# Kernel optimization log

Measured on AMD Instinct MI355X. Metric: run time of the kernel, lower is better.

Reference implementation:

```python
import math
import jax, jax.numpy as jnp
import numpy as np

B, T, E, H = 4, 4096, 512, 8
D = E // H
TOP_K = int(3 * math.log(T))  # autocorrelation_factor * log(time_length) = 24


def setup_inputs() -> dict:
    key = jax.random.key(0)
    ks = jax.random.split(key, 9)
    s = 0.02
    return {
        "hidden_states": jax.random.normal(ks[0], (B, T, E), jnp.float32),
        "Wq": jax.random.normal(ks[1], (E, E), jnp.float32) * s,
        "bq": jax.random.normal(ks[2], (E,), jnp.float32) * s,
        "Wk": jax.random.normal(ks[3], (E, E), jnp.float32) * s,
        "bk": jax.random.normal(ks[4], (E,), jnp.float32) * s,
        "Wv": jax.random.normal(ks[5], (E, E), jnp.float32) * s,
        "bv": jax.random.normal(ks[6], (E,), jnp.float32) * s,
        "Wo": jax.random.normal(ks[7], (E, E), jnp.float32) * s,
        "bo": jax.random.normal(ks[8], (E,), jnp.float32) * s,
    }


def _heads(x):
    # [B,T,E] -> [B*H,T,D] (b-major over heads, matching torch view/transpose/reshape)
    return x.reshape(B, T, H, D).transpose(0, 2, 1, 3).reshape(B * H, T, D)


def reference(hidden_states, Wq, bq, Wk, bk, Wv, bv, Wo, bo):
    q = _heads(hidden_states @ Wq.T + bq)
    k = _heads(hidden_states @ Wk.T + bk)
    v = _heads(hidden_states @ Wv.T + bv)

    # FFT-based autocorrelation: irfft(rfft(q) * conj(rfft(k)))  -> [B*H,T,D]
    qf = jnp.fft.rfft(q, n=T, axis=1)
    kf = jnp.fft.rfft(k, n=T, axis=1)
    ac = jnp.fft.irfft(qf * jnp.conj(kf), n=T, axis=1)

    # mean over heads and channels -> [B,T]; eval-mode per-batch top-k delays
    ac_mean = ac.reshape(B, H, T, D).mean(axis=(1, 3))
    top_vals, top_idx = jax.lax.top_k(ac_mean, TOP_K)      # [B,K]
    w = jax.nn.softmax(top_vals, axis=-1)                  # [B,K]

    # torch .repeat(num_heads,...) tiles batch entries: row j uses batch j % B
    w_t = jnp.tile(w, (H, 1))        # [B*H,K]
    d_t = jnp.tile(top_idx, (H, 1))  # [B*H,K]

    t = jnp.arange(T)
    agg = jnp.zeros_like(v)
    for i in range(TOP_K):
        idx = (t[None, :] + d_t[:, i:i + 1]) % T           # circular shift by -delay
        rolled = jnp.take_along_axis(v, idx[:, :, None], axis=1)
        agg = agg + w_t[:, i][:, None, None] * rolled

    out = agg.reshape(B, H, T, D).transpose(0, 2, 1, 3).reshape(B, T, E)
    return out @ Wo.T + bo
```

## Files before the change

### kernel.cpp

```cpp
#include <hip/hip_runtime.h>
#include <math.h>

#define B_ 4
#define T_ 4096
#define E_ 512
#define H_ 8
#define TOPK 24
#define FH 2049
#define FHP 2064
#define F2 2064
#define ZROWS 16512

typedef __attribute__((ext_vector_type(8))) short bf16x8;
typedef __attribute__((ext_vector_type(4))) short bf16x4;
typedef __attribute__((ext_vector_type(4))) float f32x4;

__device__ __forceinline__ unsigned short f2bf(float f) {
    unsigned u = __float_as_uint(f);
    u = (u + 0x7FFFu + ((u >> 16) & 1u)) >> 16;
    return (unsigned short)u;
}
__device__ __forceinline__ float bf2f(unsigned short h) {
    return __uint_as_float(((unsigned)h) << 16);
}

__global__ __launch_bounds__(256) void trsp_split(const float* __restrict__ hid,
                                                  float* __restrict__ Htr,
                                                  unsigned short* __restrict__ Ah)
{
    __shared__ float tile[64][68];
    const int b = blockIdx.z;
    const int t0 = blockIdx.x * 64, e0 = blockIdx.y * 64;
    const int r = threadIdx.x >> 4;
    const int c4 = (threadIdx.x & 15) * 4;
#pragma unroll
    for (int s = 0; s < 4; s++) {
        int t = t0 + r + 16 * s;
        float4 v = *(const float4*)&hid[((size_t)b * T_ + t) * E_ + e0 + c4];
        tile[r + 16 * s][c4 + 0] = v.x; tile[r + 16 * s][c4 + 1] = v.y;
        tile[r + 16 * s][c4 + 2] = v.z; tile[r + 16 * s][c4 + 3] = v.w;
        ushort4 hv = make_ushort4(f2bf(v.x), f2bf(v.y), f2bf(v.z), f2bf(v.w));
        *(ushort4*)&Ah[((size_t)b * T_ + t) * E_ + e0 + c4] = hv;
    }
    __syncthreads();
#pragma unroll
    for (int s = 0; s < 4; s++) {
        int e = e0 + r + 16 * s;
        float4 o;
        o.x = tile[c4 + 0][r + 16 * s];
        o.y = tile[c4 + 1][r + 16 * s];
        o.z = tile[c4 + 2][r + 16 * s];
        o.w = tile[c4 + 3][r + 16 * s];
        *(float4*)&Htr[((size_t)b * E_ + e) * T_ + t0 + c4] = o;
    }
}

__global__ __launch_bounds__(256) void split_w2(const float* __restrict__ wv,
                                                const float* __restrict__ wo,
                                                unsigned short* __restrict__ Wvh,
                                                unsigned short* __restrict__ Woh)
{
    const float* src = blockIdx.y ? wo : wv;
    unsigned short* dst = blockIdx.y ? Woh : Wvh;
    int i = (blockIdx.x * 256 + threadIdx.x) * 4;
    float4 v = *(const float4*)&src[i];
    *(ushort4*)&dst[i] = make_ushort4(f2bf(v.x), f2bf(v.y), f2bf(v.z), f2bf(v.w));
}

__global__ __launch_bounds__(256) void wprep_partial(const float* __restrict__ Wq,
                                                     const float* __restrict__ Wk,
                                                     float* __restrict__ Mp)
{
    __shared__ float As[8][132];
    __shared__ float Bs[8][132];
    const int j0 = blockIdx.x * 128, k0 = blockIdx.y * 128;
    const int e0 = blockIdx.z * 32;
    const int tid = threadIdx.x;
    const int tm = tid & 15, tn = tid >> 4;
    const int le = tid >> 5, lc = (tid & 31) * 4;
    float acc[8][8];
#pragma unroll
    for (int i = 0; i < 8; i++)
#pragma unroll
        for (int j = 0; j < 8; j++) acc[i][j] = 0.f;
    for (int eb = e0; eb < e0 + 32; eb += 8) {
        __syncthreads();
        *(float4*)&As[le][lc] = *(const float4*)&Wq[((size_t)(eb + le)) * 512 + k0 + lc];
        *(float4*)&Bs[le][lc] = *(const float4*)&Wk[((size_t)(eb + le)) * 512 + j0 + lc];
        __syncthreads();
#pragma unroll
        for (int e = 0; e < 8; e++) {
            float a[8], bb[8];
            *(float4*)&a[0] = *(float4*)&As[e][4 * tn];
            *(float4*)&a[4] = *(float4*)&As[e][64 + 4 * tn];
            *(float4*)&bb[0] = *(float4*)&Bs[e][4 * tm];
            *(float4*)&bb[4] = *(float4*)&Bs[e][64 + 4 * tm];
#pragma unroll
            for (int i = 0; i < 8; i++)
#pragma unroll
                for (int j = 0; j < 8; j++)
                    acc[i][j] += a[i] * bb[j];
        }
    }
    float* out = Mp + (size_t)blockIdx.z * 512 * 512;
#pragma unroll
    for (int jj = 0; jj < 8; jj++) {
        int j = j0 + ((jj < 4) ? (4 * tm + jj) : (64 + 4 * tm + jj - 4));
        float4 o0 = make_float4(acc[0][jj], acc[1][jj], acc[2][jj], acc[3][jj]);
        float4 o1 = make_float4(acc[4][jj], acc[5][jj], acc[6][jj], acc[7][jj]);
        *(float4*)&out[(size_t)j * 512 + k0 + 4 * tn] = o0;
        *(float4*)&out[(size_t)j * 512 + k0 + 64 + 4 * tn] = o1;
    }
}

__global__ __launch_bounds__(256) void reduce_split_m(const float* __restrict__ Mp,
                                                      unsigned short* __restrict__ Mth,
                                                      unsigned short* __restrict__ Mtl)
{
    int i = (blockIdx.x * 256 + threadIdx.x) * 4;
    if (i >= 512 * 512) return;
    float4 s = make_float4(0.f, 0.f, 0.f, 0.f);
#pragma unroll
    for (int z = 0; z < 16; z++) {
        float4 v = *(const float4*)&Mp[(size_t)z * 262144 + i];
        s.x += v.x; s.y += v.y; s.z += v.z; s.w += v.w;
    }
    float f[4] = {s.x, s.y, s.z, s.w};
    unsigned short hh[4], ll[4];
#pragma unroll
    for (int r = 0; r < 4; r++) {
        hh[r] = f2bf(f[r]);
        ll[r] = f2bf(f[r] - bf2f(hh[r]));
    }
    *(ushort4*)&Mth[i] = make_ushort4(hh[0], hh[1], hh[2], hh[3]);
    *(ushort4*)&Mtl[i] = make_ushort4(ll[0], ll[1], ll[2], ll[3]);
}

template<int PASSES, int AMODE, int OMODE, int HASBIAS>
__global__ __launch_bounds__(256) void mfma_gemm(const unsigned short* __restrict__ Ah,
                                                 const unsigned short* __restrict__ Al,
                                                 const unsigned short* __restrict__ Bh,
                                                 const unsigned short* __restrict__ Bl,
                                                 const float* __restrict__ bias,
                                                 void* __restrict__ Cp)
{
    constexpr int ATS = 128 * 40;
    constexpr int BTS = 64 * 40;
    constexpr int TOT = (PASSES == 3) ? 2 * (ATS + BTS) : (ATS + BTS);
    __shared__ short smem[TOT];
    short* At  = smem;
    short* Alt = smem + ((PASSES == 3) ? ATS : 0);
    short* Bt  = smem + ((PASSES == 3) ? 2 * ATS : ATS);
    short* Blt = Bt + ((PASSES == 3) ? BTS : 0);

    const int tid = threadIdx.x;
    const int m0 = blockIdx.x * 64;
    const int n0 = blockIdx.y * 128;
    const int wid = tid >> 6, lane = tid & 63;
    const int wn = wid >> 1, wm = wid & 1;
    const int lr = lane & 15, lg = lane >> 4;
    const int kb = lg * 8;

    f32x4 acc[4][2];
#pragma unroll
    for (int i = 0; i < 4; i++)
#pragma unroll
        for (int j = 0; j < 2; j++) acc[i][j] = (f32x4)0.f;

    const int r0 = tid >> 2, kp = (tid & 3) << 3;

    for (int k0 = 0; k0 < 512; k0 += 32) {
        __syncthreads();
        if (AMODE == 0) {
            size_t a0 = (size_t)(n0 + r0) * 512 + k0 + kp;
            size_t a1 = (size_t)(n0 + r0 + 64) * 512 + k0 + kp;
            *(bf16x8*)&At[r0 * 40 + kp]        = *(const bf16x8*)&Ah[a0];
            *(bf16x8*)&At[(r0 + 64) * 40 + kp] = *(const bf16x8*)&Ah[a1];
            if (PASSES == 3) {
                *(bf16x8*)&Alt[r0 * 40 + kp]        = *(const bf16x8*)&Al[a0];
                *(bf16x8*)&Alt[(r0 + 64) * 40 + kp] = *(const bf16x8*)&Al[a1];
            }
        } else {
            size_t za = (size_t)((k0 + kp) >> 2) * ZROWS;
            const size_t st = (size_t)ZROWS * 4;
            size_t a0 = (za + n0 + r0) * 4;
            size_t a1 = (za + n0 + r0 + 64) * 4;
            *(bf16x4*)&At[r0 * 40 + kp]            = *(const bf16x4*)&Ah[a0];
            *(bf16x4*)&At[r0 * 40 + kp + 4]        = *(const bf16x4*)&Ah[a0 + st];
            *(bf16x4*)&At[(r0 + 64) * 40 + kp]     = *(const bf16x4*)&Ah[a1];
            *(bf16x4*)&At[(r0 + 64) * 40 + kp + 4] = *(const bf16x4*)&Ah[a1 + st];
            if (PASSES == 3) {
                *(bf16x4*)&Alt[r0 * 40 + kp]            = *(const bf16x4*)&Al[a0];
                *(bf16x4*)&Alt[r0 * 40 + kp + 4]        = *(const bf16x4*)&Al[a0 + st];
                *(bf16x4*)&Alt[(r0 + 64) * 40 + kp]     = *(const bf16x4*)&Al[a1];
                *(bf16x4*)&Alt[(r0 + 64) * 40 + kp + 4] = *(const bf16x4*)&Al[a1 + st];
            }
        }
        size_t bb = (size_t)(m0 + r0) * 512 + k0 + kp;
        *(bf16x8*)&Bt[r0 * 40 + kp] = *(const bf16x8*)&Bh[bb];
        if (PASSES == 3)
            *(bf16x8*)&Blt[r0 * 40 + kp] = *(const bf16x8*)&Bl[bb];
        __syncthreads();

        bf16x8 a[4], b[2];
#pragma unroll
        for (int f = 0; f < 4; f++)
            a[f] = *(bf16x8*)&At[(wn * 64 + f * 16 + lr) * 40 + kb];
#pragma unroll
        for (int j = 0; j < 2; j++)
            b[j] = *(bf16x8*)&Bt[(wm * 32 + j * 16 + lr) * 40 + kb];
        if (PASSES == 3) {
            bf16x8 a2[4], b2[2];
#pragma unroll
            for (int f = 0; f < 4; f++)
                a2[f] = *(bf16x8*)&Alt[(wn * 64 + f * 16 + lr) * 40 + kb];
#pragma unroll
            for (int j = 0; j < 2; j++)
                b2[j] = *(bf16x8*)&Blt[(wm * 32 + j * 16 + lr) * 40 + kb];
#pragma unroll
            for (int i = 0; i < 4; i++)
#pragma unroll
                for (int j = 0; j < 2; j++) {
                    acc[i][j] = __builtin_amdgcn_mfma_f32_16x16x32_bf16(a[i], b[j], acc[i][j], 0, 0, 0);
                    acc[i][j] = __builtin_amdgcn_mfma_f32_16x16x32_bf16(a[i], b2[j], acc[i][j], 0, 0, 0);
                    acc[i][j] = __builtin_amdgcn_mfma_f32_16x16x32_bf16(a2[i], b[j], acc[i][j], 0, 0, 0);
                }
        } else {
#pragma unroll
            for (int i = 0; i < 4; i++)
#pragma unroll
                for (int j = 0; j < 2; j++)
                    acc[i][j] = __builtin_amdgcn_mfma_f32_16x16x32_bf16(a[i], b[j], acc[i][j], 0, 0, 0);
        }
    }

    float bs[2];
#pragma unroll
    for (int j = 0; j < 2; j++) bs[j] = HASBIAS ? bias[m0 + wm * 32 + j * 16 + lr] : 0.f;

    if (OMODE == 0) {
        float* C = (float*)Cp;
#pragma unroll
        for (int i = 0; i < 4; i++)
#pragma unroll
            for (int j = 0; j < 2; j++) {
                int m = m0 + wm * 32 + j * 16 + lr;
#pragma unroll
                for (int r = 0; r < 4; r++) {
                    int n = n0 + wn * 64 + i * 16 + lg * 4 + r;
                    C[(size_t)n * 512 + m] = acc[i][j][r] + bs[j];
                }
            }
    } else {
        unsigned short* C = (unsigned short*)Cp;
#pragma unroll
        for (int i = 0; i < 4; i++)
#pragma unroll
            for (int j = 0; j < 2; j++) {
                int m = m0 + wm * 32 + j * 16 + lr;
#pragma unroll
                for (int r = 0; r < 4; r++) {
                    int n = n0 + wn * 64 + i * 16 + lg * 4 + r;
                    C[(size_t)n * 512 + m] = f2bf(acc[i][j][r] + bs[j]);
                }
            }
    }
}

template<int SGN>
__device__ __forceinline__ void radix8(float* xr, float* xi)
{
    const float C = 0.70710678118654752440f;
    const float S = (float)SGN;
    float t0r = xr[0] + xr[4], t0i = xi[0] + xi[4];
    float t1r = xr[1] + xr[5], t1i = xi[1] + xi[5];
    float t2r = xr[2] + xr[6], t2i = xi[2] + xi[6];
    float t3r = xr[3] + xr[7], t3i = xi[3] + xi[7];
    float u0r = xr[0] - xr[4], u0i = xi[0] - xi[4];
    float a1r = xr[1] - xr[5], a1i = xi[1] - xi[5];
    float a2r = xr[2] - xr[6], a2i = xi[2] - xi[6];
    float a3r = xr[3] - xr[7], a3i = xi[3] - xi[7];
    float u1r = C * (a1r - S * a1i), u1i = C * (S * a1r + a1i);
    float u2r = -S * a2i,             u2i = S * a2r;
    float u3r = -C * (a3r + S * a3i), u3i = C * (S * a3r - a3i);
    float v0r = t0r + t2r, v0i = t0i + t2i;
    float w0r = t0r - t2r, w0i = t0i - t2i;
    float v1r = t1r + t3r, v1i = t1i + t3i;
    float w1r = -S * (t1i - t3i), w1i = S * (t1r - t3r);
    float p0r = u0r + u2r, p0i = u0i + u2i;
    float q0r = u0r - u2r, q0i = u0i - u2i;
    float p1r = u1r + u3r, p1i = u1i + u3i;
    float q1r = -S * (u1i - u3i), q1i = S * (u1r - u3r);
    xr[0] = v0r + v1r; xi[0] = v0i + v1i;
    xr[4] = v0r - v1r; xi[4] = v0i - v1i;
    xr[2] = w0r + w1r; xi[2] = w0i + w1i;
    xr[6] = w0r - w1r; xi[6] = w0i - w1i;
    xr[1] = p0r + p1r; xi[1] = p0i + p1i;
    xr[5] = p0r - p1r; xi[5] = p0i - p1i;
    xr[3] = q0r + q1r; xi[3] = q0i + q1i;
    xr[7] = q0r - q1r; xi[7] = q0i - q1i;
}

__device__ __forceinline__ void twmul(float& xr, float& xi, float wc, float ws)
{
    float a = xr, b = xi;
    xr = a * wc - b * ws;
    xi = a * ws + b * wc;
}

__device__ __forceinline__ void twiddle7(float* xr, float* xi, int n, float ang)
{
    float s1, c1;
    __sincosf(ang * (float)n, &s1, &c1);
    float wc = c1, ws = s1;
    twmul(xr[1], xi[1], wc, ws);
#pragma unroll
    for (int r = 2; r < 8; r++) {
        float nc = wc * c1 - ws * s1;
        float ns = wc * s1 + ws * c1;
        wc = nc; ws = ns;
        twmul(xr[r], xi[r], wc, ws);
    }
}

#define SW(i) ((i) + ((i) >> 3))

template<int SGN>
__device__ __forceinline__ void fft_core(float* xr, float* xi,
                                         float* lre, float* lim, int tid)
{
    const float TW = (float)SGN * 6.28318530717958647693f;
    __syncthreads();
    radix8<SGN>(xr, xi);
    twiddle7(xr, xi, tid, TW / 4096.f);
#pragma unroll
    for (int r = 0; r < 8; r++) {
        int idx = r * 512 + tid;
        lre[SW(idx)] = xr[r]; lim[SW(idx)] = xi[r];
    }
    __syncthreads();
    const int b2 = (tid >> 6) * 512, n2 = tid & 63;
#pragma unroll
    for (int s = 0; s < 8; s++) {
        int idx = b2 + n2 + s * 64;
        xr[s] = lre[SW(idx)]; xi[s] = lim[SW(idx)];
    }
    __syncthreads();
    radix8<SGN>(xr, xi);
    twiddle7(xr, xi, n2, TW / 512.f);
#pragma unroll
    for (int r = 0; r < 8; r++) {
        int idx = b2 + r * 64 + n2;
        lre[SW(idx)] = xr[r]; lim[SW(idx)] = xi[r];
    }
    __syncthreads();
    const int b3 = (tid >> 3) * 64, n3 = tid & 7;
#pragma unroll
    for (int s = 0; s < 8; s++) {
        int idx = b3 + n3 + s * 8;
        xr[s] = lre[SW(idx)]; xi[s] = lim[SW(idx)];
    }
    __syncthreads();
    radix8<SGN>(xr, xi);
    twiddle7(xr, xi, n3, TW / 64.f);
#pragma unroll
    for (int r = 0; r < 8; r++) {
        int idx = b3 + r * 8 + n3;
        lre[SW(idx)] = xr[r]; lim[SW(idx)] = xi[r];
    }
    __syncthreads();
#pragma unroll
    for (int s = 0; s < 8; s++) {
        int idx = tid * 8 + s;
        xr[s] = lre[SW(idx)]; xi[s] = lim[SW(idx)];
    }
    __syncthreads();
    radix8<SGN>(xr, xi);
    const int fr = ((tid & 7) << 6) | (((tid >> 3) & 7) << 3) | (tid >> 6);
#pragma unroll
    for (int r = 0; r < 8; r++) {
        int f = r * 512 + fr;
        lre[SW(f)] = xr[r]; lim[SW(f)] = xi[r];
    }
    __syncthreads();
}

__global__ __launch_bounds__(512) void fft_fwd_z(const float* __restrict__ Htr,
                                                 unsigned short* __restrict__ Zh,
                                                 unsigned short* __restrict__ Zl)
{
    __shared__ float lre[4608];
    __shared__ float lim[4608];
    const int bid = blockIdx.x;
    const int tid = threadIdx.x;
    const int b = bid >> 7;
    const int e0 = (bid & 127) * 4;
    const int kbi = e0 >> 2;
    unsigned uh[4][2][2], ul[4][2][2];
#pragma unroll
    for (int p = 0; p < 2; p++) {
        const float* he = Htr + ((size_t)(b * 512 + e0 + 2 * p)) * 4096;
        const float* ho = Htr + ((size_t)(b * 512 + e0 + 2 * p + 1)) * 4096;
        float xr[8], xi[8];
#pragma unroll
        for (int s = 0; s < 8; s++) {
            xr[s] = he[tid + 512 * s];
            xi[s] = ho[tid + 512 * s];
        }
        fft_core<-1>(xr, xi, lre, lim, tid);
#pragma unroll
        for (int s = 0; s < 4; s++) {
            int f = tid + 512 * s;
            int nf = (4096 - f) & 4095;
            float Ax = lre[SW(f)],  Ay = lim[SW(f)];
            float Bx = lre[SW(nf)], By = lim[SW(nf)];
            float qx = 0.5f * (Ax + Bx), qy = 0.5f * (Ay - By);
            float kx = 0.5f * (Ay + By), ky = -0.5f * (Ax - Bx);
            unsigned short h0 = f2bf(qx), h1 = f2bf(kx);
            uh[s][0][p] = (unsigned)h0 | ((unsigned)h1 << 16);
            ul[s][0][p] = (unsigned)f2bf(qx - bf2f(h0)) | ((unsigned)f2bf(kx - bf2f(h1)) << 16);
            unsigned short h2 = f2bf(qy), h3 = f2bf(ky);
            uh[s][1][p] = (unsigned)h2 | ((unsigned)h3 << 16);
            ul[s][1][p] = (unsigned)f2bf(qy - bf2f(h2)) | ((unsigned)f2bf(ky - bf2f(h3)) << 16);
        }
        if (tid == 0) {
            float Ax = lre[SW(2048)], Ay = lim[SW(2048)];
            size_t row0 = (size_t)(b * 2) * F2 + 2048;
            size_t off0 = ((size_t)kbi * ZROWS + row0) * 4 + 2 * p;
            unsigned short h = f2bf(Ax);
            Zh[off0] = h; Zl[off0] = f2bf(Ax - bf2f(h));
            unsigned short h2 = f2bf(Ay);
            Zh[off0 + 1] = h2; Zl[off0 + 1] = f2bf(Ay - bf2f(h2));
            size_t off1 = ((size_t)kbi * ZROWS + row0 + F2) * 4 + 2 * p;
            Zh[off1] = 0; Zl[off1] = 0;
            Zh[off1 + 1] = 0; Zl[off1 + 1] = 0;
        }
    }
#pragma unroll
    for (int s = 0; s < 4; s++)
#pragma unroll
        for (int c = 0; c < 2; c++) {
            size_t row = (size_t)(b * 2 + c) * F2 + tid + 512 * s;
            size_t off = ((size_t)kbi * ZROWS + row) * 4;
            ushort4 vh = make_ushort4((unsigned short)(uh[s][c][0] & 0xffff),
                                      (unsigned short)(uh[s][c][0] >> 16),
                                      (unsigned short)(uh[s][c][1] & 0xffff),
                                      (unsigned short)(uh[s][c][1] >> 16));
            ushort4 vl = make_ushort4((unsigned short)(ul[s][c][0] & 0xffff),
                                      (unsigned short)(ul[s][c][0] >> 16),
                                      (unsigned short)(ul[s][c][1] & 0xffff),
                                      (unsigned short)(ul[s][c][1] >> 16));
            *(ushort4*)&Zh[off] = vh;
            *(ushort4*)&Zl[off] = vl;
        }
}

__global__ __launch_bounds__(256) void dot_s(const float* __restrict__ Y,
                                             const unsigned short* __restrict__ Zh,
                                             const unsigned short* __restrict__ Zl,
                                             float2* __restrict__ Sp)
{
    const int f = blockIdx.x * 256 + threadIdx.x;
    const int b = blockIdx.y;
    const int gz = blockIdx.z;
    if (f > 2048) return;
    const size_t row_re = (size_t)(b * 2) * F2 + f;
    const size_t row_im = row_re + F2;
    float sre = 0.f, sim = 0.f;
    for (int kb = gz * 16; kb < gz * 16 + 16; kb++) {
        size_t zr_off = ((size_t)kb * ZROWS + row_re) * 4;
        size_t zi_off = ((size_t)kb * ZROWS + row_im) * 4;
        bf16x4 zrh = *(const bf16x4*)&Zh[zr_off];
        bf16x4 zrl = *(const bf16x4*)&Zl[zr_off];
        bf16x4 zih = *(const bf16x4*)&Zh[zi_off];
        bf16x4 zil = *(const bf16x4*)&Zl[zi_off];
        float4 yr = *(const float4*)&Y[row_re * 512 + kb * 4];
        float4 yi = *(const float4*)&Y[row_im * 512 + kb * 4];
        float yrv[4] = {yr.x, yr.y, yr.z, yr.w};
        float yiv[4] = {yi.x, yi.y, yi.z, yi.w};
#pragma unroll
        for (int j = 0; j < 4; j++) {
            float zr = bf2f((unsigned short)zrh[j]) + bf2f((unsigned short)zrl[j]);
            float zi = bf2f((unsigned short)zih[j]) + bf2f((unsigned short)zil[j]);
            sre += yrv[j] * zr + yiv[j] * zi;
            sim += yiv[j] * zr - yrv[j] * zi;
        }
    }
    Sp[((size_t)gz * 4 + b) * FHP + f] = make_float2(sre, sim);
}

__global__ __launch_bounds__(512) void ifft_kernel(const float2* __restrict__ Sp,
                                                   float* __restrict__ acm)
{
    __shared__ float lre[4608];
    __shared__ float lim[4608];
    const int b = blockIdx.x, tid = threadIdx.x;
    float xr[8], xi[8];
#pragma unroll
    for (int s = 0; s < 8; s++) {
        int idx = tid + 512 * s;
        int src = (idx <= 2048) ? idx : (4096 - idx);
        float sx = 0.f, sy = 0.f;
#pragma unroll
        for (int gz = 0; gz < 8; gz++) {
            float2 v = Sp[((size_t)gz * 4 + b) * FHP + src];
            sx += v.x; sy += v.y;
        }
        xr[s] = sx;
        xi[s] = (idx <= 2048) ? sy : -sy;
    }
    fft_core<1>(xr, xi, lre, lim, tid);
    const float scale = 1.0f / ((float)T_ * (float)E_);
#pragma unroll
    for (int s = 0; s < 8; s++) {
        int p = tid + 512 * s;
        acm[b * T_ + p] = lre[SW(p)] * scale;
    }
}

__global__ __launch_bounds__(256) void topk_kernel(const float* __restrict__ acm,
                                                   int* __restrict__ delays,
                                                   float* __restrict__ weights)
{
    __shared__ float vals[4096];
    __shared__ float bv[256];
    __shared__ int   bi[256];
    __shared__ float topv[TOPK];
    const int b = blockIdx.x, tid = threadIdx.x;
#pragma unroll
    for (int s = 0; s < 16; s++) vals[tid + 256 * s] = acm[b * T_ + tid + 256 * s];
    __syncthreads();
    for (int it = 0; it < TOPK; it++) {
        float best = -INFINITY; int bidx = 0;
#pragma unroll
        for (int s = 0; s < 16; s++) {
            int idx = tid * 16 + s;
            float v = vals[idx];
            if (v > best) { best = v; bidx = idx; }
        }
        bv[tid] = best; bi[tid] = bidx;
        __syncthreads();
        for (int off = 128; off > 0; off >>= 1) {
            if (tid < off) {
                if (bv[tid + off] > bv[tid] ||
                    (bv[tid + off] == bv[tid] && bi[tid + off] < bi[tid])) {
                    bv[tid] = bv[tid + off]; bi[tid] = bi[tid + off];
                }
            }
            __syncthreads();
        }
        if (tid == 0) {
            delays[b * TOPK + it] = bi[0];
            topv[it] = bv[0];
            vals[bi[0]] = -INFINITY;
        }
        __syncthreads();
    }
    if (tid == 0) {
        float mx = topv[0];
        float w[TOPK], sum = 0.f;
        for (int i = 0; i < TOPK; i++) { w[i] = expf(topv[i] - mx); sum += w[i]; }
        for (int i = 0; i < TOPK; i++) weights[b * TOPK + i] = w[i] / sum;
    }
}

__global__ __launch_bounds__(256) void agg_kernel(const unsigned short* __restrict__ V,
                                                  const int* __restrict__ delays,
                                                  const float* __restrict__ wts,
                                                  unsigned short* __restrict__ agg)
{
    __shared__ int   dly[B_][TOPK];
    __shared__ float wt[B_][TOPK];
    const int tid = threadIdx.x, b = blockIdx.y;
    if (tid < B_ * TOPK) {
        dly[tid / TOPK][tid % TOPK] = delays[tid];
        wt[tid / TOPK][tid % TOPK]  = wts[tid];
    }
    __syncthreads();
    const int lane = tid & 63, w = tid >> 6;
    const int t = blockIdx.x * 4 + w;
    const int e8 = lane * 8;
    const int h = e8 >> 6;
    const int c = (b * H_ + h) % B_;
    const unsigned short* Vb = V + (size_t)b * T_ * E_;
    float acc[8];
#pragma unroll
    for (int j = 0; j < 8; j++) acc[j] = 0.f;
#pragma unroll
    for (int i = 0; i < TOPK; i++) {
        int tt = (t + dly[c][i]) & (T_ - 1);
        bf16x8 v = *(const bf16x8*)&Vb[(size_t)tt * E_ + e8];
        float wg = wt[c][i];
#pragma unroll
        for (int j = 0; j < 8; j++)
            acc[j] += wg * bf2f((unsigned short)v[j]);
    }
    bf16x8 o;
#pragma unroll
    for (int j = 0; j < 8; j++) o[j] = (short)f2bf(acc[j]);
    *(bf16x8*)&agg[((size_t)b * T_ + t) * E_ + e8] = o;
}

extern "C" void kernel_launch(void* const* d_in, const int* in_sizes, int n_in,
                              void* d_out, int out_size, void* d_ws, size_t ws_size,
                              hipStream_t stream)
{
    const float* hidden = (const float*)d_in[0];
    const float* Wq = (const float*)d_in[1];
    const float* Wk = (const float*)d_in[3];
    const float* Wv = (const float*)d_in[5]; const float* bv = (const float*)d_in[6];
    const float* Wo = (const float*)d_in[7]; const float* bo = (const float*)d_in[8];

    char* ws = (char*)d_ws;
    const size_t YA_OFF  = 0;
    const size_t AH_OFF  = 33816576;
    const size_t ZH_OFF  = 50593792;
    const size_t ZL_OFF  = 67502080;
    const size_t VB_OFF  = 84410368;
    const size_t MTH_OFF = 101187584;
    const size_t MTL_OFF = 101711872;
    const size_t WVH_OFF = 102236160;
    const size_t WOH_OFF = 102760448;
    const size_t SP_OFF  = 103284736;
    const size_t ACM_OFF = 103813120;
    const size_t DEL_OFF = 103878656;
    const size_t WTS_OFF = 103879040;
    if (ws_size < 103879424) return;

    float* Htr = (float*)(ws + YA_OFF);
    float* Y   = (float*)(ws + YA_OFF);
    unsigned short* Ah  = (unsigned short*)(ws + AH_OFF);
    unsigned short* Ag  = (unsigned short*)(ws + AH_OFF);
    unsigned short* Zh  = (unsigned short*)(ws + ZH_OFF);
    unsigned short* Zl  = (unsigned short*)(ws + ZL_OFF);
    float* Mp           = (float*)(ws + VB_OFF);
    unsigned short* Vb  = (unsigned short*)(ws + VB_OFF);
    unsigned short* Mth = (unsigned short*)(ws + MTH_OFF);
    unsigned short* Mtl = (unsigned short*)(ws + MTL_OFF);
    unsigned short* Wvh = (unsigned short*)(ws + WVH_OFF);
    unsigned short* Woh = (unsigned short*)(ws + WOH_OFF);
    float2* Sp   = (float2*)(ws + SP_OFF);
    float*  acm  = (float*)(ws + ACM_OFF);
    int*    delays = (int*)(ws + DEL_OFF);
    float*  wts    = (float*)(ws + WTS_OFF);

    dim3 tg(64, 8, 4);
    trsp_split<<<tg, 256, 0, stream>>>(hidden, Htr, Ah);
    dim3 swg(256, 2);
    split_w2<<<swg, 256, 0, stream>>>(Wv, Wo, Wvh, Woh);
    dim3 mg(4, 4, 16);
    wprep_partial<<<mg, 256, 0, stream>>>(Wq, Wk, Mp);
    reduce_split_m<<<256, 256, 0, stream>>>(Mp, Mth, Mtl);

    dim3 gv(8, 128);
    mfma_gemm<1, 0, 2, 1><<<gv, 256, 0, stream>>>(Ah, Ah, Wvh, Wvh, bv, Vb);

    fft_fwd_z<<<512, 512, 0, stream>>>(Htr, Zh, Zl);

    dim3 gy(8, 129);
    mfma_gemm<3, 1, 0, 0><<<gy, 256, 0, stream>>>(Zh, Zl, Mth, Mtl, bv, Y);

    dim3 dg(9, 4, 8);
    dot_s<<<dg, 256, 0, stream>>>(Y, Zh, Zl, Sp);

    ifft_kernel<<<B_, 512, 0, stream>>>(Sp, acm);
    topk_kernel<<<B_, 256, 0, stream>>>(acm, delays, wts);
    dim3 ag(T_ / 4, B_);
    agg_kernel<<<ag, 256, 0, stream>>>(Vb, delays, wts, Ag);
    mfma_gemm<1, 0, 0, 1><<<gv, 256, 0, stream>>>(Ag, Ag, Woh, Woh, bo, (float*)d_out);
}
```

Measured before the change: 285.4 us.

## Use k-chunked operand layout with direct global-to-LDS loads, fuse V and Y GEMMs

All GEMM operands (activations, weights, Z spectra, aggregated values) are rewritten in a k-chunk-major layout of 8 bf16 per row, so GEMM tiles can be filled with global_load_lds 16-byte direct copies instead of register round-trips. The GEMM tile grows from 128x64 to 128x128 with 4x4 MFMA fragments per wave. The V projection and the 3-pass Y GEMM are merged into one launch using blockIdx.z. Producers and dot_s are updated to match the new layout. This aims to reduce LDS staging overhead and launch count, at the cost of more registers per thread and LDS layouts without padding that may cause bank conflicts.

```diff
diff --git a/kernel.cpp b/kernel.cpp
--- a/kernel.cpp
+++ b/kernel.cpp
@@ -10,9 +10,9 @@
 #define FHP 2064
 #define F2 2064
 #define ZROWS 16512
+#define NRH 16384
 
 typedef __attribute__((ext_vector_type(8))) short bf16x8;
-typedef __attribute__((ext_vector_type(4))) short bf16x4;
 typedef __attribute__((ext_vector_type(4))) float f32x4;
 
 __device__ __forceinline__ unsigned short f2bf(float f) {
@@ -23,6 +23,12 @@
 __device__ __forceinline__ float bf2f(unsigned short h) {
     return __uint_as_float(((unsigned)h) << 16);
 }
+__device__ __forceinline__ void glds16(const unsigned short* g, short* l) {
+    __builtin_amdgcn_global_load_lds(
+        (const __attribute__((address_space(1))) unsigned int*)g,
+        (__attribute__((address_space(3))) unsigned int*)l, 16, 0, 0);
+}
+
 
 __global__ __launch_bounds__(256) void trsp_split(const float* __restrict__ hid,
                                                   float* __restrict__ Htr,
@@ -40,7 +46,9 @@
         tile[r + 16 * s][c4 + 0] = v.x; tile[r + 16 * s][c4 + 1] = v.y;
         tile[r + 16 * s][c4 + 2] = v.z; tile[r + 16 * s][c4 + 3] = v.w;
         ushort4 hv = make_ushort4(f2bf(v.x), f2bf(v.y), f2bf(v.z), f2bf(v.w));
-        *(ushort4*)&Ah[((size_t)b * T_ + t) * E_ + e0 + c4] = hv;
+        int e = e0 + c4;
+        int rowg = b * T_ + t;
+        *(ushort4*)&Ah[((size_t)(e >> 3) * NRH + rowg) * 8 + (e & 7)] = hv;
     }
     __syncthreads();
 #pragma unroll
@@ -63,8 +71,10 @@
     const float* src = blockIdx.y ? wo : wv;
     unsigned short* dst = blockIdx.y ? Woh : Wvh;
     int i = (blockIdx.x * 256 + threadIdx.x) * 4;
+    int m = i >> 9, k = i & 511;
     float4 v = *(const float4*)&src[i];
-    *(ushort4*)&dst[i] = make_ushort4(f2bf(v.x), f2bf(v.y), f2bf(v.z), f2bf(v.w));
+    *(ushort4*)&dst[((size_t)(k >> 3) * 512 + m) * 8 + (k & 7)] =
+        make_ushort4(f2bf(v.x), f2bf(v.y), f2bf(v.z), f2bf(v.w));
 }
 
 __global__ __launch_bounds__(256) void wprep_partial(const float* __restrict__ Wq,
@@ -125,6 +135,7 @@
         float4 v = *(const float4*)&Mp[(size_t)z * 262144 + i];
         s.x += v.x; s.y += v.y; s.z += v.z; s.w += v.w;
     }
+    int j = i >> 9, k = i & 511;
     float f[4] = {s.x, s.y, s.z, s.w};
     unsigned short hh[4], ll[4];
 #pragma unroll
@@ -132,95 +143,68 @@
         hh[r] = f2bf(f[r]);
         ll[r] = f2bf(f[r] - bf2f(hh[r]));
     }
-    *(ushort4*)&Mth[i] = make_ushort4(hh[0], hh[1], hh[2], hh[3]);
-    *(ushort4*)&Mtl[i] = make_ushort4(ll[0], ll[1], ll[2], ll[3]);
-}
-
-template<int PASSES, int AMODE, int OMODE, int HASBIAS>
-__global__ __launch_bounds__(256) void mfma_gemm(const unsigned short* __restrict__ Ah,
-                                                 const unsigned short* __restrict__ Al,
-                                                 const unsigned short* __restrict__ Bh,
-                                                 const unsigned short* __restrict__ Bl,
-                                                 const float* __restrict__ bias,
-                                                 void* __restrict__ Cp)
-{
-    constexpr int ATS = 128 * 40;
-    constexpr int BTS = 64 * 40;
-    constexpr int TOT = (PASSES == 3) ? 2 * (ATS + BTS) : (ATS + BTS);
-    __shared__ short smem[TOT];
-    short* At  = smem;
-    short* Alt = smem + ((PASSES == 3) ? ATS : 0);
-    short* Bt  = smem + ((PASSES == 3) ? 2 * ATS : ATS);
-    short* Blt = Bt + ((PASSES == 3) ? BTS : 0);
-
+    size_t o = ((size_t)(k >> 3) * 512 + j) * 8 + (k & 7);
+    *(ushort4*)&Mth[o] = make_ushort4(hh[0], hh[1], hh[2], hh[3]);
+    *(ushort4*)&Mtl[o] = make_ushort4(ll[0], ll[1], ll[2], ll[3]);
+}
+
+template<int PASSES, int OMODE, int HASBIAS>
+__device__ __forceinline__ void gemm_body(const unsigned short* __restrict__ Ah,
+                                          const unsigned short* __restrict__ Al, int nrA,
+                                          const unsigned short* __restrict__ Bh,
+                                          const unsigned short* __restrict__ Bl,
+                                          const float* __restrict__ bias,
+                                          void* __restrict__ Cp,
+                                          int m0, int n0, short* smem)
+{
     const int tid = threadIdx.x;
-    const int m0 = blockIdx.x * 64;
-    const int n0 = blockIdx.y * 128;
     const int wid = tid >> 6, lane = tid & 63;
     const int wn = wid >> 1, wm = wid & 1;
     const int lr = lane & 15, lg = lane >> 4;
-    const int kb = lg * 8;
-
-    f32x4 acc[4][2];
+
+    f32x4 acc[4][4];
 #pragma unroll
     for (int i = 0; i < 4; i++)
 #pragma unroll
-        for (int j = 0; j < 2; j++) acc[i][j] = (f32x4)0.f;
-
-    const int r0 = tid >> 2, kp = (tid & 3) << 3;
-
-    for (int k0 = 0; k0 < 512; k0 += 32) {
+        for (int j = 0; j < 4; j++) acc[i][j] = (f32x4)0.f;
+
+    constexpr int SEGW = (PASSES == 3) ? 8 : 4;
+
+    for (int kc0 = 0; kc0 < 64; kc0 += 4) {
         __syncthreads();
-        if (AMODE == 0) {
-            size_t a0 = (size_t)(n0 + r0) * 512 + k0 + kp;
-            size_t a1 = (size_t)(n0 + r0 + 64) * 512 + k0 + kp;
-            *(bf16x8*)&At[r0 * 40 + kp]        = *(const bf16x8*)&Ah[a0];
-            *(bf16x8*)&At[(r0 + 64) * 40 + kp] = *(const bf16x8*)&Ah[a1];
-            if (PASSES == 3) {
-                *(bf16x8*)&Alt[r0 * 40 + kp]        = *(const bf16x8*)&Al[a0];
-                *(bf16x8*)&Alt[(r0 + 64) * 40 + kp] = *(const bf16x8*)&Al[a1];
+#pragma unroll
+        for (int s = 0; s < SEGW; s++) {
+            const int sg = wid * SEGW + s;
+            const int tile = sg >> 3;
+            const int seg = sg & 7;
+            const int c = seg >> 1, h = seg & 1;
+            const unsigned short* bp;
+            size_t ro;
+            if (tile == 0)      { bp = Ah; ro = (size_t)(kc0 + c) * (size_t)nrA + n0 + h * 64; }
+            else if (tile == 1) { bp = Bh; ro = (size_t)(kc0 + c) * 512 + m0 + h * 64; }
+            else if (tile == 2) { bp = Al; ro = (size_t)(kc0 + c) * (size_t)nrA + n0 + h * 64; }
+            else                { bp = Bl; ro = (size_t)(kc0 + c) * 512 + m0 + h * 64; }
+            glds16(bp + ro * 8 + (size_t)lane * 8, smem + tile * 4096 + seg * 512);
+        }
+        __syncthreads();
+
+        bf16x8 a[4], b[4];
+#pragma unroll
+        for (int f = 0; f < 4; f++) {
+            a[f] = *(bf16x8*)&smem[       (lg * 128 + wn * 64 + f * 16 + lr) * 8];
+            b[f] = *(bf16x8*)&smem[4096 + (lg * 128 + wm * 64 + f * 16 + lr) * 8];
+        }
+        if (PASSES == 3) {
+            bf16x8 a2[4], b2[4];
+#pragma unroll
+            for (int f = 0; f < 4; f++) {
+                a2[f] = *(bf16x8*)&smem[8192  + (lg * 128 + wn * 64 + f * 16 + lr) * 8];
+                b2[f] = *(bf16x8*)&smem[12288 + (lg * 128 + wm * 64 + f * 16 + lr) * 8];
             }
-        } else {
-            size_t za = (size_t)((k0 + kp) >> 2) * ZROWS;
-            const size_t st = (size_t)ZROWS * 4;
-            size_t a0 = (za + n0 + r0) * 4;
-            size_t a1 = (za + n0 + r0 + 64) * 4;
-            *(bf16x4*)&At[r0 * 40 + kp]            = *(const bf16x4*)&Ah[a0];
-            *(bf16x4*)&At[r0 * 40 + kp + 4]        = *(const bf16x4*)&Ah[a0 + st];
-            *(bf16x4*)&At[(r0 + 64) * 40 + kp]     = *(const bf16x4*)&Ah[a1];
-            *(bf16x4*)&At[(r0 + 64) * 40 + kp + 4] = *(const bf16x4*)&Ah[a1 + st];
-            if (PASSES == 3) {
-                *(bf16x4*)&Alt[r0 * 40 + kp]            = *(const bf16x4*)&Al[a0];
-                *(bf16x4*)&Alt[r0 * 40 + kp + 4]        = *(const bf16x4*)&Al[a0 + st];
-                *(bf16x4*)&Alt[(r0 + 64) * 40 + kp]     = *(const bf16x4*)&Al[a1];
-                *(bf16x4*)&Alt[(r0 + 64) * 40 + kp + 4] = *(const bf16x4*)&Al[a1 + st];
-            }
-        }
-        size_t bb = (size_t)(m0 + r0) * 512 + k0 + kp;
-        *(bf16x8*)&Bt[r0 * 40 + kp] = *(const bf16x8*)&Bh[bb];
-        if (PASSES == 3)
-            *(bf16x8*)&Blt[r0 * 40 + kp] = *(const bf16x8*)&Bl[bb];
-        __syncthreads();
-
-        bf16x8 a[4], b[2];
-#pragma unroll
-        for (int f = 0; f < 4; f++)
-            a[f] = *(bf16x8*)&At[(wn * 64 + f * 16 + lr) * 40 + kb];
-#pragma unroll
-        for (int j = 0; j < 2; j++)
-            b[j] = *(bf16x8*)&Bt[(wm * 32 + j * 16 + lr) * 40 + kb];
-        if (PASSES == 3) {
-            bf16x8 a2[4], b2[2];
-#pragma unroll
-            for (int f = 0; f < 4; f++)
-                a2[f] = *(bf16x8*)&Alt[(wn * 64 + f * 16 + lr) * 40 + kb];
-#pragma unroll
-            for (int j = 0; j < 2; j++)
-                b2[j] = *(bf16x8*)&Blt[(wm * 32 + j * 16 + lr) * 40 + kb];
 #pragma unroll
             for (int i = 0; i < 4; i++)
 #pragma unroll
-                for (int j = 0; j < 2; j++) {
+                for (int j = 0; j < 4; j++) {
                     acc[i][j] = __builtin_amdgcn_mfma_f32_16x16x32_bf16(a[i], b[j], acc[i][j], 0, 0, 0);
                     acc[i][j] = __builtin_amdgcn_mfma_f32_16x16x32_bf16(a[i], b2[j], acc[i][j], 0, 0, 0);
                     acc[i][j] = __builtin_amdgcn_mfma_f32_16x16x32_bf16(a2[i], b[j], acc[i][j], 0, 0, 0);
@@ -229,22 +213,22 @@
 #pragma unroll
             for (int i = 0; i < 4; i++)
 #pragma unroll
-                for (int j = 0; j < 2; j++)
+                for (int j = 0; j < 4; j++)
                     acc[i][j] = __builtin_amdgcn_mfma_f32_16x16x32_bf16(a[i], b[j], acc[i][j], 0, 0, 0);
         }
     }
 
-    float bs[2];
-#pragma unroll
-    for (int j = 0; j < 2; j++) bs[j] = HASBIAS ? bias[m0 + wm * 32 + j * 16 + lr] : 0.f;
+    float bs[4];
+#pragma unroll
+    for (int j = 0; j < 4; j++) bs[j] = HASBIAS ? bias[m0 + wm * 64 + j * 16 + lr] : 0.f;
 
     if (OMODE == 0) {
         float* C = (float*)Cp;
 #pragma unroll
         for (int i = 0; i < 4; i++)
 #pragma unroll
-            for (int j = 0; j < 2; j++) {
-                int m = m0 + wm * 32 + j * 16 + lr;
+            for (int j = 0; j < 4; j++) {
+                int m = m0 + wm * 64 + j * 16 + lr;
 #pragma unroll
                 for (int r = 0; r < 4; r++) {
                     int n = n0 + wn * 64 + i * 16 + lg * 4 + r;
@@ -256,8 +240,8 @@
 #pragma unroll
         for (int i = 0; i < 4; i++)
 #pragma unroll
-            for (int j = 0; j < 2; j++) {
-                int m = m0 + wm * 32 + j * 16 + lr;
+            for (int j = 0; j < 4; j++) {
+                int m = m0 + wm * 64 + j * 16 + lr;
 #pragma unroll
                 for (int r = 0; r < 4; r++) {
                     int n = n0 + wn * 64 + i * 16 + lg * 4 + r;
@@ -265,6 +249,36 @@
                 }
             }
     }
+}
+
+__global__ __launch_bounds__(256) void fused_vy(const unsigned short* __restrict__ Ah,
+                                                const unsigned short* __restrict__ Wvh,
+                                                const float* __restrict__ bv,
+                                                unsigned short* __restrict__ Vb,
+                                                const unsigned short* __restrict__ Zh,
+                                                const unsigned short* __restrict__ Zl,
+                                                const unsigned short* __restrict__ Mth,
+                                                const unsigned short* __restrict__ Mtl,
+                                                float* __restrict__ Y)
+{
+    __shared__ short smem[16384];
+    const int m0 = blockIdx.x * 128;
+    const int n0 = blockIdx.y * 128;
+    if (blockIdx.z == 0) {
+        if (blockIdx.y >= 128) return;
+        gemm_body<1, 2, 1>(Ah, Ah, NRH, Wvh, Wvh, bv, Vb, m0, n0, smem);
+    } else {
+        gemm_body<3, 0, 0>(Zh, Zl, ZROWS, Mth, Mtl, nullptr, Y, m0, n0, smem);
+    }
+}
+
+__global__ __launch_bounds__(256) void o_gemm(const unsigned short* __restrict__ Ag,
+                                              const unsigned short* __restrict__ Woh,
+                                              const float* __restrict__ bo,
+                                              float* __restrict__ C)
+{
+    __shared__ short smem[8192];
+    gemm_body<1, 0, 1>(Ag, Ag, NRH, Woh, Woh, bo, C, blockIdx.x * 128, blockIdx.y * 128, smem);
 }
 
 template<int SGN>
@@ -395,7 +409,6 @@
     const int tid = threadIdx.x;
     const int b = bid >> 7;
     const int e0 = (bid & 127) * 4;
-    const int kbi = e0 >> 2;
     unsigned uh[4][2][2], ul[4][2][2];
 #pragma unroll
     for (int p = 0; p < 2; p++) {
@@ -424,16 +437,17 @@
             ul[s][1][p] = (unsigned)f2bf(qy - bf2f(h2)) | ((unsigned)f2bf(ky - bf2f(h3)) << 16);
         }
         if (tid == 0) {
-            float Ax = lre[SW(2048)], Ay = lim[SW(2048)];
+            float vals[2] = {lre[SW(2048)], lim[SW(2048)]};
             size_t row0 = (size_t)(b * 2) * F2 + 2048;
-            size_t off0 = ((size_t)kbi * ZROWS + row0) * 4 + 2 * p;
-            unsigned short h = f2bf(Ax);
-            Zh[off0] = h; Zl[off0] = f2bf(Ax - bf2f(h));
-            unsigned short h2 = f2bf(Ay);
-            Zh[off0 + 1] = h2; Zl[off0 + 1] = f2bf(Ay - bf2f(h2));
-            size_t off1 = ((size_t)kbi * ZROWS + row0 + F2) * 4 + 2 * p;
-            Zh[off1] = 0; Zl[off1] = 0;
-            Zh[off1 + 1] = 0; Zl[off1 + 1] = 0;
+#pragma unroll
+            for (int q = 0; q < 2; q++) {
+                int e = e0 + 2 * p + q;
+                size_t o0 = ((size_t)(e >> 3) * ZROWS + row0) * 8 + (e & 7);
+                unsigned short h = f2bf(vals[q]);
+                Zh[o0] = h; Zl[o0] = f2bf(vals[q] - bf2f(h));
+                size_t o1 = ((size_t)(e >> 3) * ZROWS + row0 + F2) * 8 + (e & 7);
+                Zh[o1] = 0; Zl[o1] = 0;
+            }
         }
     }
 #pragma unroll
@@ -441,7 +455,7 @@
 #pragma unroll
         for (int c = 0; c < 2; c++) {
             size_t row = (size_t)(b * 2 + c) * F2 + tid + 512 * s;
-            size_t off = ((size_t)kbi * ZROWS + row) * 4;
+            size_t off = ((size_t)(e0 >> 3) * ZROWS + row) * 8 + (e0 & 7);
             ushort4 vh = make_ushort4((unsigned short)(uh[s][c][0] & 0xffff),
                                       (unsigned short)(uh[s][c][0] >> 16),
                                       (unsigned short)(uh[s][c][1] & 0xffff),
@@ -467,19 +481,19 @@
     const size_t row_re = (size_t)(b * 2) * F2 + f;
     const size_t row_im = row_re + F2;
     float sre = 0.f, sim = 0.f;
-    for (int kb = gz * 16; kb < gz * 16 + 16; kb++) {
-        size_t zr_off = ((size_t)kb * ZROWS + row_re) * 4;
-        size_t zi_off = ((size_t)kb * ZROWS + row_im) * 4;
-        bf16x4 zrh = *(const bf16x4*)&Zh[zr_off];
-        bf16x4 zrl = *(const bf16x4*)&Zl[zr_off];
-        bf16x4 zih = *(const bf16x4*)&Zh[zi_off];
-        bf16x4 zil = *(const bf16x4*)&Zl[zi_off];
-        float4 yr = *(const float4*)&Y[row_re * 512 + kb * 4];
-        float4 yi = *(const float4*)&Y[row_im * 512 + kb * 4];
-        float yrv[4] = {yr.x, yr.y, yr.z, yr.w};
-        float yiv[4] = {yi.x, yi.y, yi.z, yi.w};
-#pragma unroll
-        for (int j = 0; j < 4; j++) {
+    for (int c = gz * 8; c < gz * 8 + 8; c++) {
+        bf16x8 zrh = *(const bf16x8*)&Zh[((size_t)c * ZROWS + row_re) * 8];
+        bf16x8 zrl = *(const bf16x8*)&Zl[((size_t)c * ZROWS + row_re) * 8];
+        bf16x8 zih = *(const bf16x8*)&Zh[((size_t)c * ZROWS + row_im) * 8];
+        bf16x8 zil = *(const bf16x8*)&Zl[((size_t)c * ZROWS + row_im) * 8];
+        float4 yr0 = *(const float4*)&Y[row_re * 512 + c * 8];
+        float4 yr1 = *(const float4*)&Y[row_re * 512 + c * 8 + 4];
+        float4 yi0 = *(const float4*)&Y[row_im * 512 + c * 8];
+        float4 yi1 = *(const float4*)&Y[row_im * 512 + c * 8 + 4];
+        float yrv[8] = {yr0.x, yr0.y, yr0.z, yr0.w, yr1.x, yr1.y, yr1.z, yr1.w};
+        float yiv[8] = {yi0.x, yi0.y, yi0.z, yi0.w, yi1.x, yi1.y, yi1.z, yi1.w};
+#pragma unroll
+        for (int j = 0; j < 8; j++) {
             float zr = bf2f((unsigned short)zrh[j]) + bf2f((unsigned short)zrl[j]);
             float zi = bf2f((unsigned short)zih[j]) + bf2f((unsigned short)zil[j]);
             sre += yrv[j] * zr + yiv[j] * zi;
@@ -598,7 +612,8 @@
     bf16x8 o;
 #pragma unroll
     for (int j = 0; j < 8; j++) o[j] = (short)f2bf(acc[j]);
-    *(bf16x8*)&agg[((size_t)b * T_ + t) * E_ + e8] = o;
+    int rowg = b * T_ + t;
+    *(bf16x8*)&agg[((size_t)(e8 >> 3) * NRH + rowg) * 8] = o;
 }
 
 extern "C" void kernel_launch(void* const* d_in, const int* in_sizes, int n_in,
@@ -652,13 +667,10 @@
     wprep_partial<<<mg, 256, 0, stream>>>(Wq, Wk, Mp);
     reduce_split_m<<<256, 256, 0, stream>>>(Mp, Mth, Mtl);
 
-    dim3 gv(8, 128);
-    mfma_gemm<1, 0, 2, 1><<<gv, 256, 0, stream>>>(Ah, Ah, Wvh, Wvh, bv, Vb);
-
     fft_fwd_z<<<512, 512, 0, stream>>>(Htr, Zh, Zl);
 
-    dim3 gy(8, 129);
-    mfma_gemm<3, 1, 0, 0><<<gy, 256, 0, stream>>>(Zh, Zl, Mth, Mtl, bv, Y);
+    dim3 gf(4, 129, 2);
+    fused_vy<<<gf, 256, 0, stream>>>(Ah, Wvh, bv, Vb, Zh, Zl, Mth, Mtl, Y);
 
     dim3 dg(9, 4, 8);
     dot_s<<<dg, 256, 0, stream>>>(Y, Zh, Zl, Sp);
@@ -667,5 +679,6 @@
     topk_kernel<<<B_, 256, 0, stream>>>(acm, delays, wts);
     dim3 ag(T_ / 4, B_);
     agg_kernel<<<ag, 256, 0, stream>>>(Vb, delays, wts, Ag);
-    mfma_gemm<1, 0, 0, 1><<<gv, 256, 0, stream>>>(Ag, Ag, Woh, Woh, bo, (float*)d_out);
-}
+    dim3 go(4, 128);
+    o_gemm<<<go, 256, 0, stream>>>(Ag, Woh, bo, (float*)d_out);
+}
```

New measurement: 251.9 us. 1.13x faster.
